# Optimization experiments

Measured on AMD Instinct MI355X. Metric: run time of the kernel, lower is better.

The kernel has to match this reference:

```python
import jax, jax.numpy as jnp
import numpy as np

D_IN = 1024
D_OUT = 1024
NUM_HEADS = 16
HEAD_DIM = D_OUT // NUM_HEADS


def setup_inputs() -> dict:
    key = jax.random.key(0)
    ks = jax.random.split(key, 6)
    s = 0.02
    return {
        "x": jax.random.normal(ks[0], (4, 2048, D_IN), dtype=jnp.float32),
        "Wq": jax.random.normal(ks[1], (D_IN, D_OUT), dtype=jnp.float32) * s,
        "Wk": jax.random.normal(ks[2], (D_IN, D_OUT), dtype=jnp.float32) * s,
        "Wv": jax.random.normal(ks[3], (D_IN, D_OUT), dtype=jnp.float32) * s,
        "Wo": jax.random.normal(ks[4], (D_OUT, D_OUT), dtype=jnp.float32) * s,
        "bo": jax.random.normal(ks[5], (D_OUT,), dtype=jnp.float32) * s,
    }


def reference(x, Wq, Wk, Wv, Wo, bo):
    B, S, _ = x.shape
    # QKV projections (no bias), split into heads: [B, H, S, Dh]
    def split_heads(t):
        return t.reshape(B, S, NUM_HEADS, HEAD_DIM).transpose(0, 2, 1, 3)

    q = split_heads(x @ Wq)
    k = split_heads(x @ Wk)
    v = split_heads(x @ Wv)

    # causal scores [B, H, S, S]; note: original masks BEFORE scaling,
    # but -inf is scale-invariant so softmax(scores/sqrt(d)) with mask is identical.
    scores = jnp.einsum("bhqd,bhkd->bhqk", q, k) / jnp.sqrt(jnp.asarray(HEAD_DIM, x.dtype))
    causal = jnp.tril(jnp.ones((S, S), dtype=bool))
    scores = jnp.where(causal, scores, -jnp.inf)
    attn = jax.nn.softmax(scores, axis=-1)
    # dropout p=0.0 -> identity
    ctx = jnp.einsum("bhqk,bhkd->bhqd", attn, v)  # [B, H, S, Dh]
    ctx = ctx.transpose(0, 2, 1, 3).reshape(B, S, D_OUT)
    return ctx @ Wo + bo
```

## Files before the change

kernel.cpp:

```cpp
#include <hip/hip_runtime.h>
#include <hip/hip_bf16.h>
#include <math.h>


typedef __attribute__((ext_vector_type(8))) short short8;
typedef __attribute__((ext_vector_type(4))) float f32x4;

#define MFMA_BF16(a, b, c) __builtin_amdgcn_mfma_f32_16x16x32_bf16((a), (b), (c), 0, 0, 0)

__device__ __forceinline__ void gld_lds16(const void* g, void* l) {
  __builtin_amdgcn_global_load_lds((const __attribute__((address_space(1))) void*)g,
                                   (__attribute__((address_space(3))) void*)l, 16, 0, 0);
}

__global__ void prep_kernel(const float* __restrict__ x, __hip_bfloat16* __restrict__ xb,
                            const float* __restrict__ W0, const float* __restrict__ W1,
                            const float* __restrict__ W2, const float* __restrict__ W3,
                            __hip_bfloat16* __restrict__ T0, __hip_bfloat16* __restrict__ T1,
                            __hip_bfloat16* __restrict__ T2, __hip_bfloat16* __restrict__ T3) {
  const int bid = blockIdx.x, tid = threadIdx.x;
  if (bid < 8192) {
    int i = bid * 256 + tid;
    float4 v = ((const float4*)x)[i];
    __align__(8) __hip_bfloat16 tmp[4] = {__float2bfloat16(v.x), __float2bfloat16(v.y),
                                          __float2bfloat16(v.z), __float2bfloat16(v.w)};
    ((ushort4*)xb)[i] = *(const ushort4*)tmp;
  } else {
    int zz = bid - 8192;
    int z = zz >> 10, rem = zz & 1023;
    const float* W = (z == 0) ? W0 : (z == 1) ? W1 : (z == 2) ? W2 : W3;
    __hip_bfloat16* Wt = (z == 0) ? T0 : (z == 1) ? T1 : (z == 2) ? T2 : T3;
    __shared__ float tile[32][33];
    int tx = tid & 31, ty = tid >> 5;
    int n0 = (rem & 31) * 32, k0 = (rem >> 5) * 32;
#pragma unroll
    for (int i = 0; i < 4; ++i)
      tile[ty + i * 8][tx] = W[(size_t)(k0 + ty + i * 8) * 1024 + n0 + tx];
    __syncthreads();
#pragma unroll
    for (int i = 0; i < 4; ++i)
      Wt[(size_t)(n0 + ty + i * 8) * 1024 + k0 + tx] = __float2bfloat16(tile[tx][ty + i * 8]);
  }
}

__global__ __launch_bounds__(256, 2) void gemm_qkv(
    const __hip_bfloat16* __restrict__ A, const __hip_bfloat16* __restrict__ Bt,
    __hip_bfloat16* __restrict__ q, __hip_bfloat16* __restrict__ k,
    __hip_bfloat16* __restrict__ vT) {
  __shared__ __align__(16) __hip_bfloat16 As[128 * 64];
  __shared__ __align__(16) __hip_bfloat16 Bs[128 * 64];
  const int tid = threadIdx.x;
  const int lane = tid & 63, wid = tid >> 6;
  const int quad = lane >> 4, l16 = lane & 15;
  const int part = blockIdx.x >> 3;
  const int n0 = (blockIdx.x & 7) * 128;
  const int gn0 = part * 1024 + n0;
  const int m0 = blockIdx.y * 128;
  const int wm = (wid & 1) * 64, wn = (wid >> 1) * 64;
  const int swz = l16 & 7;

  f32x4 acc[4][4] = {};

  for (int k0 = 0; k0 < 1024; k0 += 64) {
    __syncthreads();
#pragma unroll
    for (int i = 0; i < 4; ++i) {
      int sbase = __builtin_amdgcn_readfirstlane(wid * 256 + i * 64);
      int s = sbase + lane;
      int row = s >> 3;
      int ch = (s & 7) ^ (row & 7);
      gld_lds16(A + (size_t)(m0 + row) * 1024 + k0 + ch * 8, &As[sbase * 8]);
      gld_lds16(Bt + (size_t)(gn0 + row) * 1024 + k0 + ch * 8, &Bs[sbase * 8]);
    }
    __syncthreads();

    short8 af[4][2], bfr[4][2];
#pragma unroll
    for (int t = 0; t < 4; ++t)
#pragma unroll
      for (int kc = 0; kc < 2; ++kc) {
        int chp = (kc * 4 + quad) ^ swz;
        af[t][kc]  = *(const short8*)&As[(wm + t * 16 + l16) * 64 + chp * 8];
        bfr[t][kc] = *(const short8*)&Bs[(wn + t * 16 + l16) * 64 + chp * 8];
      }
#pragma unroll
    for (int kc = 0; kc < 2; ++kc)
#pragma unroll
      for (int mt = 0; mt < 4; ++mt)
#pragma unroll
        for (int nt = 0; nt < 4; ++nt)
          acc[mt][nt] = MFMA_BF16(af[mt][kc], bfr[nt][kc], acc[mt][nt]);
  }

  const float CSCL = 0.18033688011112042f;
  if (part < 2) {
    __hip_bfloat16* C = (part == 0) ? q : k;
    const float scl = (part == 0) ? CSCL : 1.0f;
#pragma unroll
    for (int mt = 0; mt < 4; ++mt)
#pragma unroll
      for (int nt = 0; nt < 4; ++nt) {
        int row = m0 + wm + mt * 16 + quad * 4;
        int col = n0 + wn + nt * 16 + l16;
#pragma unroll
        for (int r = 0; r < 4; ++r)
          C[(size_t)(row + r) * 1024 + col] = __float2bfloat16(acc[mt][nt][r] * scl);
      }
  } else {
#pragma unroll
    for (int mt = 0; mt < 4; ++mt)
#pragma unroll
      for (int nt = 0; nt < 4; ++nt) {
        int row = m0 + wm + mt * 16 + quad * 4;
        int nn = n0 + wn + nt * 16 + l16;
        __align__(8) __hip_bfloat16 p4[4];
#pragma unroll
        for (int r = 0; r < 4; ++r) p4[r] = __float2bfloat16(acc[mt][nt][r]);
        *(ushort4*)(vT + (size_t)nn * 8192 + row) = *(const ushort4*)p4;
      }
  }
}

__global__ __launch_bounds__(256, 2) void gemm_bt_f32out(
    const __hip_bfloat16* __restrict__ A, const __hip_bfloat16* __restrict__ Bt,
    float* __restrict__ C, const float* __restrict__ bias, int M, int N, int K) {
  __shared__ __align__(16) __hip_bfloat16 As[128 * 64];
  __shared__ __align__(16) __hip_bfloat16 Bs[128 * 64];
  const int tid = threadIdx.x;
  const int lane = tid & 63, wid = tid >> 6;
  const int quad = lane >> 4, l16 = lane & 15;
  const int m0 = blockIdx.y * 128, n0 = blockIdx.x * 128;
  const int wm = (wid & 1) * 64, wn = (wid >> 1) * 64;
  const int swz = l16 & 7;

  f32x4 acc[4][4] = {};

  for (int k0 = 0; k0 < K; k0 += 64) {
    __syncthreads();
#pragma unroll
    for (int i = 0; i < 4; ++i) {
      int sbase = __builtin_amdgcn_readfirstlane(wid * 256 + i * 64);
      int s = sbase + lane;
      int row = s >> 3;
      int ch = (s & 7) ^ (row & 7);
      gld_lds16(A + (size_t)(m0 + row) * K + k0 + ch * 8, &As[sbase * 8]);
      gld_lds16(Bt + (size_t)(n0 + row) * K + k0 + ch * 8, &Bs[sbase * 8]);
    }
    __syncthreads();

    short8 af[4][2], bfr[4][2];
#pragma unroll
    for (int t = 0; t < 4; ++t)
#pragma unroll
      for (int kc = 0; kc < 2; ++kc) {
        int chp = (kc * 4 + quad) ^ swz;
        af[t][kc]  = *(const short8*)&As[(wm + t * 16 + l16) * 64 + chp * 8];
        bfr[t][kc] = *(const short8*)&Bs[(wn + t * 16 + l16) * 64 + chp * 8];
      }
#pragma unroll
    for (int kc = 0; kc < 2; ++kc)
#pragma unroll
      for (int mt = 0; mt < 4; ++mt)
#pragma unroll
        for (int nt = 0; nt < 4; ++nt)
          acc[mt][nt] = MFMA_BF16(af[mt][kc], bfr[nt][kc], acc[mt][nt]);
  }

#pragma unroll
  for (int mt = 0; mt < 4; ++mt)
#pragma unroll
    for (int nt = 0; nt < 4; ++nt) {
      int row = m0 + wm + mt * 16 + quad * 4;
      int col = n0 + wn + nt * 16 + l16;
      float b = bias[col];
#pragma unroll
      for (int r = 0; r < 4; ++r)
        C[(size_t)(row + r) * N + col] = acc[mt][nt][r] + b;
    }
}

__global__ __launch_bounds__(256, 2) void attn_kernel(
    const __hip_bfloat16* __restrict__ Q, const __hip_bfloat16* __restrict__ Km,
    const __hip_bfloat16* __restrict__ vT, __hip_bfloat16* __restrict__ ctx) {
  const int bid = blockIdx.x;
  const int p = bid & 7, h = (bid >> 3) & 15, b = bid >> 7;
  const size_t rbase = (size_t)b * 2048;
  const int tid = threadIdx.x, lane = tid & 63, wid = tid >> 6;
  const int quad = lane >> 4, l16 = lane & 15;

  __shared__ __align__(16) __hip_bfloat16 Ks[64 * 72];
  __shared__ __align__(16) __hip_bfloat16 Vs[64 * 72];
  __shared__ __align__(16) __hip_bfloat16 Ps[4][32 * 76];

  const float NEG_BIG = -1e30f;

#pragma unroll 1
  for (int sub = 0; sub < 2; ++sub) {
    const int qt = sub ? (15 - p) : p;
    const int q0 = qt * 128;

    short8 qf[2][2];
#pragma unroll
    for (int mt = 0; mt < 2; ++mt)
#pragma unroll
      for (int kc = 0; kc < 2; ++kc)
        qf[mt][kc] = *(const short8*)(Q + (rbase + q0 + wid * 32 + mt * 16 + l16) * 1024 +
                                      h * 64 + kc * 32 + quad * 8);

    f32x4 o[2][4] = {};
    f32x4 lp[2] = {};
    const int wave_max_row = q0 + wid * 32 + 31;
    const int ktiles = q0 / 64 + 2;

#pragma unroll 1
    for (int kt = 0; kt < ktiles; ++kt) {
      const int kbase = kt * 64;
      __syncthreads();
      {
#pragma unroll
        for (int i = 0; i < 2; ++i) {
          int s = tid + i * 256;
          int krow = s >> 3, ch = s & 7;
          *(short8*)&Ks[krow * 72 + ch * 8] =
              *(const short8*)(Km + (rbase + kbase + krow) * 1024 + h * 64 + ch * 8);
        }
      }
      {
#pragma unroll
        for (int i = 0; i < 2; ++i) {
          int s = tid + i * 256;
          int d = s >> 3, ch = s & 7;
          *(short8*)&Vs[d * 72 + ch * 8] =
              *(const short8*)(vT + (size_t)(h * 64 + d) * 8192 + rbase + kbase + ch * 8);
        }
      }
      __syncthreads();

      if (kbase <= wave_max_row) {
        short8 kf[4][2];
#pragma unroll
        for (int nt = 0; nt < 4; ++nt)
#pragma unroll
          for (int kc = 0; kc < 2; ++kc)
            kf[nt][kc] = *(const short8*)&Ks[(nt * 16 + l16) * 72 + kc * 32 + quad * 8];
        f32x4 s[2][4];
#pragma unroll
        for (int mt = 0; mt < 2; ++mt)
#pragma unroll
          for (int nt = 0; nt < 4; ++nt) {
            f32x4 sv = {0.f, 0.f, 0.f, 0.f};
            sv = MFMA_BF16(qf[mt][0], kf[nt][0], sv);
            sv = MFMA_BF16(qf[mt][1], kf[nt][1], sv);
            s[mt][nt] = sv;
          }
        if (kbase + 63 > q0 + wid * 32) {
#pragma unroll
          for (int mt = 0; mt < 2; ++mt)
#pragma unroll
            for (int nt = 0; nt < 4; ++nt)
#pragma unroll
              for (int r = 0; r < 4; ++r) {
                int row = q0 + wid * 32 + mt * 16 + quad * 4 + r;
                int col = kbase + nt * 16 + l16;
                if (col > row) s[mt][nt][r] = NEG_BIG;
              }
        }
#pragma unroll
        for (int mt = 0; mt < 2; ++mt) {
#pragma unroll
          for (int nt = 0; nt < 4; ++nt)
#pragma unroll
            for (int r = 0; r < 4; ++r) {
              float pv = __builtin_amdgcn_exp2f(s[mt][nt][r]);
              s[mt][nt][r] = pv;
              lp[mt][r] += pv;
            }
#pragma unroll
          for (int nt = 0; nt < 4; ++nt)
#pragma unroll
            for (int r = 0; r < 4; ++r)
              Ps[wid][(mt * 16 + quad * 4 + r) * 76 + nt * 16 + l16] =
                  __float2bfloat16(s[mt][nt][r]);
        }
        short8 pa[2][2], vf[4][2];
#pragma unroll
        for (int mt = 0; mt < 2; ++mt)
#pragma unroll
          for (int ch = 0; ch < 2; ++ch)
            pa[mt][ch] = *(const short8*)&Ps[wid][(mt * 16 + l16) * 76 + ch * 32 + quad * 8];
#pragma unroll
        for (int dt = 0; dt < 4; ++dt)
#pragma unroll
          for (int ch = 0; ch < 2; ++ch)
            vf[dt][ch] = *(const short8*)&Vs[(dt * 16 + l16) * 72 + ch * 32 + quad * 8];
#pragma unroll
        for (int mt = 0; mt < 2; ++mt)
#pragma unroll
          for (int dt = 0; dt < 4; ++dt) {
            o[mt][dt] = MFMA_BF16(pa[mt][0], vf[dt][0], o[mt][dt]);
            o[mt][dt] = MFMA_BF16(pa[mt][1], vf[dt][1], o[mt][dt]);
          }
      }
    }

#pragma unroll
    for (int mt = 0; mt < 2; ++mt) {
#pragma unroll
      for (int msk = 1; msk <= 8; msk <<= 1)
#pragma unroll
        for (int r = 0; r < 4; ++r)
          lp[mt][r] += __shfl_xor(lp[mt][r], msk, 64);
      float inv[4];
#pragma unroll
      for (int r = 0; r < 4; ++r) inv[r] = 1.f / lp[mt][r];
#pragma unroll
      for (int dt = 0; dt < 4; ++dt)
#pragma unroll
        for (int r = 0; r < 4; ++r)
          ctx[(rbase + q0 + wid * 32 + mt * 16 + quad * 4 + r) * 1024 + h * 64 + dt * 16 + l16] =
              __float2bfloat16(o[mt][dt][r] * inv[r]);
    }
  }
}

extern "C" void kernel_launch(void* const* d_in, const int* in_sizes, int n_in,
                              void* d_out, int out_size, void* d_ws, size_t ws_size,
                              hipStream_t stream) {
  const float* x  = (const float*)d_in[0];
  const float* Wq = (const float*)d_in[1];
  const float* Wk = (const float*)d_in[2];
  const float* Wv = (const float*)d_in[3];
  const float* Wo = (const float*)d_in[4];
  const float* bo = (const float*)d_in[5];
  float* out = (float*)d_out;

  char* ws = (char*)d_ws;
  const size_t MB = 1024ull * 1024ull;
  __hip_bfloat16* q   = (__hip_bfloat16*)(ws);
  __hip_bfloat16* k   = (__hip_bfloat16*)(ws + 16 * MB);
  __hip_bfloat16* vT  = (__hip_bfloat16*)(ws + 32 * MB);
  __hip_bfloat16* woT = (__hip_bfloat16*)(ws + 48 * MB);
  __hip_bfloat16* ctx = q;

  char* outc = (char*)d_out;
  __hip_bfloat16* xb    = (__hip_bfloat16*)(outc);
  __hip_bfloat16* wcatT = (__hip_bfloat16*)(outc + 16 * MB);

  prep_kernel<<<8192 + 4096, 256, 0, stream>>>(
      x, xb, Wq, Wk, Wv, Wo,
      wcatT, wcatT + 1024 * 1024, wcatT + 2048 * 1024, woT);

  gemm_qkv<<<dim3(24, 64), 256, 0, stream>>>(xb, wcatT, q, k, vT);

  attn_kernel<<<512, 256, 0, stream>>>(q, k, vT, ctx);

  gemm_bt_f32out<<<dim3(8, 64), 256, 0, stream>>>(ctx, woT, out, bo, 8192, 1024, 1024);
}
```

Before: 241.4 us.

## Split attention waves into 2x2 query/key grid with LDS reduction of partial outputs

Reorganizes the four waves of the attention block from four 32-row query strips into a 2x2 grid: each wave handles 64 query rows against half (32 columns) of each 64-key tile. K fragments per wave halve and each loaded K/V fragment feeds more MFMAs. Partial outputs and row sums from the key-half waves are reduced through a new 36KB fp32 LDS buffer before normalization. This adds a block barrier and more LDS, which may reduce occupancy at 2 blocks/CU. It also makes causal skipping coarser (64-row granularity per wave), which can add wasted work.

```diff
diff --git a/kernel.cpp b/kernel.cpp
--- a/kernel.cpp
+++ b/kernel.cpp
@@ -187,10 +187,12 @@
   const size_t rbase = (size_t)b * 2048;
   const int tid = threadIdx.x, lane = tid & 63, wid = tid >> 6;
   const int quad = lane >> 4, l16 = lane & 15;
+  const int qh = wid >> 1, kh = wid & 1;
 
   __shared__ __align__(16) __hip_bfloat16 Ks[64 * 72];
   __shared__ __align__(16) __hip_bfloat16 Vs[64 * 72];
-  __shared__ __align__(16) __hip_bfloat16 Ps[4][32 * 76];
+  __shared__ __align__(16) __hip_bfloat16 Ps[4][64 * 36];
+  __shared__ __align__(16) float Os[128 * 72];
 
   const float NEG_BIG = -1e30f;
 
@@ -198,18 +200,18 @@
   for (int sub = 0; sub < 2; ++sub) {
     const int qt = sub ? (15 - p) : p;
     const int q0 = qt * 128;
-
-    short8 qf[2][2];
-#pragma unroll
-    for (int mt = 0; mt < 2; ++mt)
+    const int wrow0 = q0 + qh * 64;
+
+    short8 qf[4][2];
+#pragma unroll
+    for (int mt = 0; mt < 4; ++mt)
 #pragma unroll
       for (int kc = 0; kc < 2; ++kc)
-        qf[mt][kc] = *(const short8*)(Q + (rbase + q0 + wid * 32 + mt * 16 + l16) * 1024 +
+        qf[mt][kc] = *(const short8*)(Q + (rbase + wrow0 + mt * 16 + l16) * 1024 +
                                       h * 64 + kc * 32 + quad * 8);
 
-    f32x4 o[2][4] = {};
-    f32x4 lp[2] = {};
-    const int wave_max_row = q0 + wid * 32 + 31;
+    f32x4 o[4][4] = {};
+    f32x4 lp[4] = {};
     const int ktiles = q0 / 64 + 2;
 
 #pragma unroll 1
@@ -236,39 +238,40 @@
       }
       __syncthreads();
 
-      if (kbase <= wave_max_row) {
-        short8 kf[4][2];
-#pragma unroll
-        for (int nt = 0; nt < 4; ++nt)
+      const int wkbase = kbase + kh * 32;
+      if (wkbase <= wrow0 + 63) {
+        short8 kf[2][2];
+#pragma unroll
+        for (int nt = 0; nt < 2; ++nt)
 #pragma unroll
           for (int kc = 0; kc < 2; ++kc)
-            kf[nt][kc] = *(const short8*)&Ks[(nt * 16 + l16) * 72 + kc * 32 + quad * 8];
-        f32x4 s[2][4];
-#pragma unroll
-        for (int mt = 0; mt < 2; ++mt)
-#pragma unroll
-          for (int nt = 0; nt < 4; ++nt) {
+            kf[nt][kc] = *(const short8*)&Ks[(kh * 32 + nt * 16 + l16) * 72 + kc * 32 + quad * 8];
+        f32x4 s[4][2];
+#pragma unroll
+        for (int mt = 0; mt < 4; ++mt)
+#pragma unroll
+          for (int nt = 0; nt < 2; ++nt) {
             f32x4 sv = {0.f, 0.f, 0.f, 0.f};
             sv = MFMA_BF16(qf[mt][0], kf[nt][0], sv);
             sv = MFMA_BF16(qf[mt][1], kf[nt][1], sv);
             s[mt][nt] = sv;
           }
-        if (kbase + 63 > q0 + wid * 32) {
-#pragma unroll
-          for (int mt = 0; mt < 2; ++mt)
-#pragma unroll
-            for (int nt = 0; nt < 4; ++nt)
+        if (wkbase + 31 > wrow0) {
+#pragma unroll
+          for (int mt = 0; mt < 4; ++mt)
+#pragma unroll
+            for (int nt = 0; nt < 2; ++nt)
 #pragma unroll
               for (int r = 0; r < 4; ++r) {
-                int row = q0 + wid * 32 + mt * 16 + quad * 4 + r;
-                int col = kbase + nt * 16 + l16;
+                int row = wrow0 + mt * 16 + quad * 4 + r;
+                int col = wkbase + nt * 16 + l16;
                 if (col > row) s[mt][nt][r] = NEG_BIG;
               }
         }
 #pragma unroll
-        for (int mt = 0; mt < 2; ++mt) {
-#pragma unroll
-          for (int nt = 0; nt < 4; ++nt)
+        for (int mt = 0; mt < 4; ++mt) {
+#pragma unroll
+          for (int nt = 0; nt < 2; ++nt)
 #pragma unroll
             for (int r = 0; r < 4; ++r) {
               float pv = __builtin_amdgcn_exp2f(s[mt][nt][r]);
@@ -276,49 +279,69 @@
               lp[mt][r] += pv;
             }
 #pragma unroll
-          for (int nt = 0; nt < 4; ++nt)
+          for (int nt = 0; nt < 2; ++nt)
 #pragma unroll
             for (int r = 0; r < 4; ++r)
-              Ps[wid][(mt * 16 + quad * 4 + r) * 76 + nt * 16 + l16] =
+              Ps[wid][(mt * 16 + quad * 4 + r) * 36 + nt * 16 + l16] =
                   __float2bfloat16(s[mt][nt][r]);
         }
-        short8 pa[2][2], vf[4][2];
-#pragma unroll
-        for (int mt = 0; mt < 2; ++mt)
-#pragma unroll
-          for (int ch = 0; ch < 2; ++ch)
-            pa[mt][ch] = *(const short8*)&Ps[wid][(mt * 16 + l16) * 76 + ch * 32 + quad * 8];
+        short8 pa[4], vf[4];
+#pragma unroll
+        for (int mt = 0; mt < 4; ++mt)
+          pa[mt] = *(const short8*)&Ps[wid][(mt * 16 + l16) * 36 + quad * 8];
 #pragma unroll
         for (int dt = 0; dt < 4; ++dt)
-#pragma unroll
-          for (int ch = 0; ch < 2; ++ch)
-            vf[dt][ch] = *(const short8*)&Vs[(dt * 16 + l16) * 72 + ch * 32 + quad * 8];
-#pragma unroll
-        for (int mt = 0; mt < 2; ++mt)
-#pragma unroll
-          for (int dt = 0; dt < 4; ++dt) {
-            o[mt][dt] = MFMA_BF16(pa[mt][0], vf[dt][0], o[mt][dt]);
-            o[mt][dt] = MFMA_BF16(pa[mt][1], vf[dt][1], o[mt][dt]);
-          }
-      }
-    }
-
-#pragma unroll
-    for (int mt = 0; mt < 2; ++mt) {
+          vf[dt] = *(const short8*)&Vs[(dt * 16 + l16) * 72 + kh * 32 + quad * 8];
+#pragma unroll
+        for (int mt = 0; mt < 4; ++mt)
+#pragma unroll
+          for (int dt = 0; dt < 4; ++dt)
+            o[mt][dt] = MFMA_BF16(pa[mt], vf[dt], o[mt][dt]);
+      }
+    }
+
+#pragma unroll
+    for (int mt = 0; mt < 4; ++mt)
 #pragma unroll
       for (int msk = 1; msk <= 8; msk <<= 1)
 #pragma unroll
         for (int r = 0; r < 4; ++r)
           lp[mt][r] += __shfl_xor(lp[mt][r], msk, 64);
-      float inv[4];
-#pragma unroll
-      for (int r = 0; r < 4; ++r) inv[r] = 1.f / lp[mt][r];
-#pragma unroll
-      for (int dt = 0; dt < 4; ++dt)
-#pragma unroll
-        for (int r = 0; r < 4; ++r)
-          ctx[(rbase + q0 + wid * 32 + mt * 16 + quad * 4 + r) * 1024 + h * 64 + dt * 16 + l16] =
-              __float2bfloat16(o[mt][dt][r] * inv[r]);
+
+    if (kh == 1) {
+#pragma unroll
+      for (int mt = 0; mt < 4; ++mt) {
+#pragma unroll
+        for (int dt = 0; dt < 4; ++dt)
+#pragma unroll
+          for (int r = 0; r < 4; ++r)
+            Os[(qh * 64 + mt * 16 + quad * 4 + r) * 72 + dt * 16 + l16] = o[mt][dt][r];
+        if (l16 == 0)
+#pragma unroll
+          for (int r = 0; r < 4; ++r)
+            Os[(qh * 64 + mt * 16 + quad * 4 + r) * 72 + 64] = lp[mt][r];
+      }
+    }
+    __syncthreads();
+    if (kh == 0) {
+#pragma unroll
+      for (int mt = 0; mt < 4; ++mt) {
+        float inv[4];
+#pragma unroll
+        for (int r = 0; r < 4; ++r) {
+          int row = qh * 64 + mt * 16 + quad * 4 + r;
+          inv[r] = 1.f / (lp[mt][r] + Os[row * 72 + 64]);
+        }
+#pragma unroll
+        for (int dt = 0; dt < 4; ++dt)
+#pragma unroll
+          for (int r = 0; r < 4; ++r) {
+            int row = qh * 64 + mt * 16 + quad * 4 + r;
+            float ov = o[mt][dt][r] + Os[row * 72 + dt * 16 + l16];
+            ctx[(rbase + q0 + row) * 1024 + h * 64 + dt * 16 + l16] =
+                __float2bfloat16(ov * inv[r]);
+          }
+      }
     }
   }
 }
```

Result: slower. 256.2 us (+6.2%).
